# Performance work log

Measured on AMD Instinct MI355X. Metric: run time of the kernel, lower is better.

## Reference

```python
import jax, jax.numpy as jnp
import numpy as np


def _gcn_layer(h, src, dst, W, b, norm_src, norm_dst, n_nodes):
    # DGL GraphConv with norm='both': D_out^{-1/2} -> sum-aggregate -> D_in^{-1/2} -> XW + b
    m = (h * norm_src[:, None])[src]                       # [E, d] gather
    agg = jax.ops.segment_sum(m, dst, num_segments=n_nodes)  # [N, d] scatter-add
    return agg * norm_dst[:, None] @ W + b


def reference(features, src, dst, W1, b1, W2, b2):
    n_nodes = features.shape[0]
    ones = jnp.ones(src.shape[0], dtype=features.dtype)
    deg_out = jax.ops.segment_sum(ones, src, num_segments=n_nodes)
    deg_in = jax.ops.segment_sum(ones, dst, num_segments=n_nodes)
    # DGL clamps degrees to min 1 before the -1/2 power
    norm_src = jnp.clip(deg_out, 1.0, None) ** -0.5
    norm_dst = jnp.clip(deg_in, 1.0, None) ** -0.5

    h = jax.nn.relu(_gcn_layer(features, src, dst, W1, b1, norm_src, norm_dst, n_nodes))
    h = jax.nn.relu(_gcn_layer(h, src, dst, W2, b2, norm_src, norm_dst, n_nodes))
    return h


def setup_inputs() -> dict:
    key = jax.random.key(0)
    k1, k2, k3, k4, k5 = jax.random.split(key, 5)
    N, E, D = 50000, 600000, 128
    scale = 1.0 / np.sqrt(D)
    return {
        "features": jax.random.normal(k1, (N, D), dtype=jnp.float32),
        "src": jax.random.randint(k2, (E,), 0, N, dtype=jnp.int32),
        "dst": jax.random.randint(k3, (E,), 0, N, dtype=jnp.int32),
        "W1": jax.random.normal(k4, (D, D), dtype=jnp.float32) * scale,
        "b1": jnp.zeros((D,), dtype=jnp.float32),
        "W2": jax.random.normal(k5, (D, D), dtype=jnp.float32) * scale,
        "b2": jnp.zeros((D,), dtype=jnp.float32),
    }
```

## Files before the change

kernel.cpp:

```cpp
#include <hip/hip_runtime.h>

#define DIM 128
#define NCH 8
#define CH  22
#define HB  (NCH*CH)
#define HWORDS 25088
#define WSTR 136

typedef __attribute__((ext_vector_type(8))) short b8;
typedef __attribute__((ext_vector_type(4))) float f4;
typedef __attribute__((ext_vector_type(8))) unsigned short u16x8;

static __device__ __forceinline__ unsigned short f2bf(float f) {
    unsigned u = __float_as_uint(f);
    u += 0x7fffu + ((u >> 16) & 1u);
    return (unsigned short)(u >> 16);
}
static __device__ __forceinline__ float bf2f(unsigned short b) {
    return __uint_as_float((unsigned)b << 16);
}

__global__ __launch_bounds__(256) void k_hist(const int* __restrict__ src,
                                              const int* __restrict__ dst,
                                              unsigned short* __restrict__ local,
                                              unsigned* __restrict__ hist_in,
                                              unsigned* __restrict__ hist_out,
                                              int E, int W2p, int slice) {
    __shared__ unsigned h[HWORDS];
    const int t = threadIdx.x;
    const int b = blockIdx.x;
    const int e0 = b * slice;
    const int e1 = min(e0 + slice, E);
    const int W4 = W2p >> 2;
    uint4* h4 = (uint4*)h;

    for (int w = t; w < W4; w += 256) h4[w] = make_uint4(0u, 0u, 0u, 0u);
    __syncthreads();
    for (int e = e0 + t; e < e1; e += 256) {
        int d = dst[e];
        unsigned sh = (unsigned)(d & 1) * 16u;
        unsigned old = atomicAdd(&h[d >> 1], 1u << sh);
        local[e] = (unsigned short)((old >> sh) & 0xffffu);
    }
    __syncthreads();
    uint4* oin = (uint4*)(hist_in + (size_t)b * W2p);
    for (int w = t; w < W4; w += 256) { oin[w] = h4[w]; h4[w] = make_uint4(0u, 0u, 0u, 0u); }
    __syncthreads();
    for (int e = e0 + t; e < e1; e += 256) {
        int s = src[e];
        atomicAdd(&h[s >> 1], 1u << ((unsigned)(s & 1) * 16u));
    }
    __syncthreads();
    uint4* oout = (uint4*)(hist_out + (size_t)b * W2p);
    for (int w = t; w < W4; w += 256) oout[w] = h4[w];
}

__global__ __launch_bounds__(256) void k_colscan1(unsigned* __restrict__ hist_in,
                                                  const unsigned* __restrict__ hist_out,
                                                  unsigned* __restrict__ aux_in,
                                                  unsigned* __restrict__ aux_out,
                                                  int W2, int W2p) {
    int w = blockIdx.x * 256 + threadIdx.x;
    if (w >= W2) return;
    int ch = blockIdx.y;
    size_t base = (size_t)ch * CH * W2p + w;
    unsigned run = 0;
    #pragma unroll
    for (int b = 0; b < CH; ++b) {
        unsigned* p = hist_in + base + (size_t)b * W2p;
        unsigned x = *p;
        *p = run;
        run += x;
    }
    aux_in[(size_t)ch * W2p + w] = run;
    unsigned run2 = 0;
    #pragma unroll
    for (int b = 0; b < CH; ++b) run2 += hist_out[base + (size_t)b * W2p];
    aux_out[(size_t)ch * W2p + w] = run2;
}

__global__ __launch_bounds__(256) void k_colscan2(unsigned* __restrict__ aux_in,
                                                  const unsigned* __restrict__ aux_out,
                                                  int* __restrict__ cnt,
                                                  int* __restrict__ deg_out,
                                                  int* __restrict__ bsum,
                                                  int W2, int W2p, int N) {
    __shared__ int wsum[4];
    int w = blockIdx.x * 256 + threadIdx.x;
    unsigned run = 0, run2 = 0;
    if (w < W2) {
        #pragma unroll
        for (int ch = 0; ch < NCH; ++ch) {
            unsigned x = aux_in[(size_t)ch * W2p + w];
            aux_in[(size_t)ch * W2p + w] = run;
            run += x;
            run2 += aux_out[(size_t)ch * W2p + w];
        }
        int n0 = w * 2, n1 = n0 + 1;
        cnt[n0] = (int)(run & 0xffffu);
        deg_out[n0] = (int)(run2 & 0xffffu);
        if (n1 < N) {
            cnt[n1] = (int)(run >> 16);
            deg_out[n1] = (int)(run2 >> 16);
        } else {
            run &= 0xffffu;
        }
    }
    int tot = (int)(run & 0xffffu) + (int)(run >> 16);
    #pragma unroll
    for (int off = 32; off > 0; off >>= 1) tot += __shfl_down(tot, off, 64);
    int lane = threadIdx.x & 63, wave = threadIdx.x >> 6;
    if (lane == 0) wsum[wave] = tot;
    __syncthreads();
    if (threadIdx.x == 0)   bsum[2 * blockIdx.x]     = wsum[0] + wsum[1];
    if (threadIdx.x == 128) bsum[2 * blockIdx.x + 1] = wsum[2] + wsum[3];
}

__global__ __launch_bounds__(256) void k_edge_pass_fb(const int* __restrict__ src,
                                                      const int* __restrict__ dst,
                                                      int* __restrict__ deg_out,
                                                      int* __restrict__ cnt,
                                                      int* __restrict__ local_fb, int E) {
    int e = blockIdx.x * 256 + threadIdx.x;
    if (e < E) {
        atomicAdd(&deg_out[src[e]], 1);
        local_fb[e] = atomicAdd(&cnt[dst[e]], 1);
    }
}

__global__ __launch_bounds__(256) void k_block_reduce(const int* __restrict__ deg,
                                                      int* __restrict__ bsum, int N) {
    __shared__ int wsum[4];
    int i = blockIdx.x * 256 + threadIdx.x;
    int x = (i < N) ? deg[i] : 0;
    #pragma unroll
    for (int off = 32; off > 0; off >>= 1) x += __shfl_down(x, off, 64);
    int lane = threadIdx.x & 63, wave = threadIdx.x >> 6;
    if (lane == 0) wsum[wave] = x;
    __syncthreads();
    if (threadIdx.x == 0) bsum[blockIdx.x] = wsum[0] + wsum[1] + wsum[2] + wsum[3];
}

__global__ __launch_bounds__(256) void k_scan_final(const int* __restrict__ cnt,
                                                    const int* __restrict__ deg_out,
                                                    const int* __restrict__ bsum,
                                                    int* __restrict__ row_off,
                                                    float* __restrict__ norm_src,
                                                    float* __restrict__ norm_dst, int N) {
    __shared__ int wsum[4];
    __shared__ int base_s;
    const int t = threadIdx.x;
    const int lane = t & 63, wave = t >> 6;

    int pre = 0;
    for (int i = t; i < blockIdx.x; i += 256) pre += bsum[i];
    #pragma unroll
    for (int off = 32; off > 0; off >>= 1) pre += __shfl_down(pre, off, 64);
    if (lane == 0) wsum[wave] = pre;
    __syncthreads();
    if (t == 0) base_s = wsum[0] + wsum[1] + wsum[2] + wsum[3];
    __syncthreads();
    const int bpre_v = base_s;

    int i = blockIdx.x * 256 + t;
    int x = (i < N) ? cnt[i] : 0;
    int orig = x;
    #pragma unroll
    for (int off = 1; off < 64; off <<= 1) {
        int y = __shfl_up(x, off, 64);
        if (lane >= off) x += y;
    }
    if (lane == 63) wsum[wave] = x;
    __syncthreads();
    if (t == 0) {
        int s = 0;
        for (int w = 0; w < 4; ++w) { int tt = wsum[w]; wsum[w] = s; s += tt; }
    }
    __syncthreads();
    x += wsum[wave] + bpre_v;
    if (i < N) {
        row_off[i] = x - orig;
        int di = orig < 1 ? 1 : orig;
        norm_dst[i] = rsqrtf((float)di);
        int dov = deg_out[i]; if (dov < 1) dov = 1;
        norm_src[i] = rsqrtf((float)dov);
    }
    if (i == N - 1) row_off[N] = x;
}

__global__ __launch_bounds__(256) void k_fill_cast_prep(
        const int* __restrict__ src, const int* __restrict__ dst,
        const int* __restrict__ row_off,
        const unsigned short* __restrict__ local,
        const int* __restrict__ local_fb,
        const unsigned* __restrict__ hist_in,
        const unsigned* __restrict__ aux_in,
        int* __restrict__ csr_src,
        const float* __restrict__ feat, const float* __restrict__ norm_src,
        unsigned short* __restrict__ fbf,
        const float* __restrict__ W1, const float* __restrict__ W2,
        unsigned short* __restrict__ w1hi, unsigned short* __restrict__ w1lo,
        unsigned short* __restrict__ w2hi, unsigned short* __restrict__ w2lo,
        int E, int W2p, int slice, int eb, int cb, int pb, int n4) {
    int bx = blockIdx.x;
    if (bx < eb) {
        int e = bx * 256 + threadIdx.x;
        if (e < E) {
            int d = dst[e];
            int pos = row_off[d];
            if (hist_in) {
                int b = e / slice;
                int ch = b / CH;
                unsigned sh = (unsigned)(d & 1) * 16u;
                unsigned bo = (hist_in[(size_t)b * W2p + (d >> 1)] >> sh) & 0xffffu;
                unsigned cbs = (aux_in[(size_t)ch * W2p + (d >> 1)] >> sh) & 0xffffu;
                pos += (int)bo + (int)cbs + (int)local[e];
            } else {
                pos += local_fb[e];
            }
            csr_src[pos] = src[e];
        }
    } else if (bx < eb + cb) {
        int i = (bx - eb) * 256 + threadIdx.x;
        if (i < n4) {
            float4 v = ((const float4*)feat)[i];
            float ns = norm_src[i >> 5];
            ushort4 o;
            o.x = f2bf(v.x * ns); o.y = f2bf(v.y * ns);
            o.z = f2bf(v.z * ns); o.w = f2bf(v.w * ns);
            ((ushort4*)fbf)[i] = o;
        }
    } else {
        int b = bx - eb - cb;
        const float* W; unsigned short *Hi, *Lo;
        if (b < pb) { W = W1; Hi = w1hi; Lo = w1lo; } else { W = W2; Hi = w2hi; Lo = w2lo; b -= pb; }
        int e = b * 256 + threadIdx.x;
        if (e < DIM * DIM) {
            int k = e >> 7, c = e & 127;
            float w = W[e];
            unsigned short hi = f2bf(w);
            unsigned short lo = f2bf(w - bf2f(hi));
            Hi[c * DIM + k] = hi;
            Lo[c * DIM + k] = lo;
        }
    }
}

__global__ __launch_bounds__(256) void k_spmm(const unsigned short* __restrict__ hb,
                                              const int* __restrict__ csr_src,
                                              const int* __restrict__ row_off,
                                              const float* __restrict__ norm_dst,
                                              unsigned short* __restrict__ aggbf, int N) {
    int t = blockIdx.x * 256 + threadIdx.x;
    int node = t >> 4;
    int lane = t & 15;
    if (node >= N) return;
    int beg = row_off[node], end = row_off[node + 1];
    float a0[8] = {0.f, 0.f, 0.f, 0.f, 0.f, 0.f, 0.f, 0.f};
    float a1[8] = {0.f, 0.f, 0.f, 0.f, 0.f, 0.f, 0.f, 0.f};
    int i = beg;
    for (; i + 4 <= end; i += 4) {
        int s0 = csr_src[i], s1 = csr_src[i + 1], s2 = csr_src[i + 2], s3 = csr_src[i + 3];
        u16x8 u0 = *((const u16x8*)(hb + (size_t)s0 * DIM) + lane);
        u16x8 u1 = *((const u16x8*)(hb + (size_t)s1 * DIM) + lane);
        u16x8 u2 = *((const u16x8*)(hb + (size_t)s2 * DIM) + lane);
        u16x8 u3 = *((const u16x8*)(hb + (size_t)s3 * DIM) + lane);
        #pragma unroll
        for (int j = 0; j < 8; ++j) {
            a0[j] += bf2f(u0[j]);
            a1[j] += bf2f(u1[j]);
            a0[j] += bf2f(u2[j]);
            a1[j] += bf2f(u3[j]);
        }
    }
    for (; i < end; ++i) {
        int s0 = csr_src[i];
        u16x8 u0 = *((const u16x8*)(hb + (size_t)s0 * DIM) + lane);
        #pragma unroll
        for (int j = 0; j < 8; ++j) a0[j] += bf2f(u0[j]);
    }
    float nd = norm_dst[node];
    u16x8 o;
    #pragma unroll
    for (int j = 0; j < 8; ++j) o[j] = f2bf((a0[j] + a1[j]) * nd);
    *((u16x8*)(aggbf + (size_t)node * DIM) + lane) = o;
}

__global__ __launch_bounds__(256, 2) void k_gemm_mfma(
        const unsigned short* __restrict__ A,
        const unsigned short* __restrict__ Wt_hi,
        const unsigned short* __restrict__ Wt_lo,
        const float* __restrict__ bias,
        const float* __restrict__ postscale,
        float* __restrict__ outf, unsigned short* __restrict__ outbf, int N) {
    __shared__ unsigned short WH[DIM * WSTR];
    __shared__ unsigned short WL[DIM * WSTR];

    const int t = threadIdx.x;
    #pragma unroll
    for (int i = 0; i < 8; ++i) {
        int e = (t + i * 256) * 8;
        int c = e >> 7, k = e & 127;
        *(float4*)(WH + c * WSTR + k) = *(const float4*)(Wt_hi + e);
        *(float4*)(WL + c * WSTR + k) = *(const float4*)(Wt_lo + e);
    }
    __syncthreads();

    const int wv = t >> 6;
    const int l = t & 63;
    const int m = l & 15;
    const int quad = l >> 4;
    const int row_t0 = blockIdx.x * 128 + wv * 32;

    f4 acc[2][8];
    #pragma unroll
    for (int rt = 0; rt < 2; ++rt)
        #pragma unroll
        for (int ct = 0; ct < 8; ++ct)
            acc[rt][ct] = (f4){0.f, 0.f, 0.f, 0.f};

    int r0 = row_t0 + m;      if (r0 >= N) r0 = N - 1;
    int r1 = row_t0 + 16 + m; if (r1 >= N) r1 = N - 1;

    #pragma unroll
    for (int ks = 0; ks < 4; ++ks) {
        int koff = ks * 32 + quad * 8;
        b8 a0 = *(const b8*)(A + (size_t)r0 * DIM + koff);
        b8 a1 = *(const b8*)(A + (size_t)r1 * DIM + koff);
        #pragma unroll
        for (int ct = 0; ct < 8; ++ct) {
            int c = ct * 16 + m;
            b8 bh = *(const b8*)(WH + c * WSTR + koff);
            b8 bl = *(const b8*)(WL + c * WSTR + koff);
            acc[0][ct] = __builtin_amdgcn_mfma_f32_16x16x32_bf16(a0, bh, acc[0][ct], 0, 0, 0);
            acc[0][ct] = __builtin_amdgcn_mfma_f32_16x16x32_bf16(a0, bl, acc[0][ct], 0, 0, 0);
            acc[1][ct] = __builtin_amdgcn_mfma_f32_16x16x32_bf16(a1, bh, acc[1][ct], 0, 0, 0);
            acc[1][ct] = __builtin_amdgcn_mfma_f32_16x16x32_bf16(a1, bl, acc[1][ct], 0, 0, 0);
        }
    }

    #pragma unroll
    for (int rt = 0; rt < 2; ++rt) {
        int rowb = row_t0 + rt * 16 + quad * 4;
        #pragma unroll
        for (int r = 0; r < 4; ++r) {
            int gr = rowb + r;
            if (gr < N) {
                float s = postscale ? postscale[gr] : 1.f;
                #pragma unroll
                for (int ct = 0; ct < 8; ++ct) {
                    int col = ct * 16 + m;
                    float v = fmaxf(acc[rt][ct][r] + bias[col], 0.f) * s;
                    if (outbf) outbf[(size_t)gr * DIM + col] = f2bf(v);
                    else       outf[(size_t)gr * DIM + col] = v;
                }
            }
        }
    }
}

static inline size_t align_up(size_t x, size_t a) { return (x + a - 1) & ~(a - 1); }

extern "C" void kernel_launch(void* const* d_in, const int* in_sizes, int n_in,
                              void* d_out, int out_size, void* d_ws, size_t ws_size,
                              hipStream_t stream) {
    const float* features = (const float*)d_in[0];
    const int*   src      = (const int*)d_in[1];
    const int*   dst      = (const int*)d_in[2];
    const float* W1       = (const float*)d_in[3];
    const float* b1       = (const float*)d_in[4];
    const float* W2       = (const float*)d_in[5];
    const float* b2       = (const float*)d_in[6];
    float* out = (float*)d_out;

    const int N = in_sizes[0] / DIM;
    const int E = in_sizes[1];
    const int B = (N + 255) / 256;
    const int W2w = (N + 1) >> 1;
    const int W2p = (W2w + 3) & ~3;
    const int slice = (E + HB - 1) / HB;
    const int cs_blocks = (W2w + 255) / 256;

    size_t nodeb = align_up((size_t)N * 4, 256);
    char* p = (char*)d_ws;
    int*   deg_out  = (int*)p;                      p += nodeb;
    int*   cnt      = (int*)p;                      p += nodeb;
    float* norm_src = (float*)p;                    p += nodeb;
    float* norm_dst = (float*)p;                    p += nodeb;
    int*   row_off  = (int*)p;                      p += align_up((size_t)(N + 1) * 4, 256);
    int*   bsum     = (int*)p;                      p += align_up((size_t)(2 * cs_blocks) * 4, 256);
    int*   csr_src  = (int*)p;                      p += align_up((size_t)E * 4, 256);
    char*  big      = p;                            p += 2 * (size_t)N * DIM * 4;
    unsigned short* w1hi = (unsigned short*)p;      p += (size_t)DIM * DIM * 2;
    unsigned short* w1lo = (unsigned short*)p;      p += (size_t)DIM * DIM * 2;
    unsigned short* w2hi = (unsigned short*)p;      p += (size_t)DIM * DIM * 2;
    unsigned short* w2lo = (unsigned short*)p;      p += (size_t)DIM * DIM * 2;
    unsigned short* aggbf = (unsigned short*)big;
    unsigned short* h1bf  = (unsigned short*)(big + (size_t)N * DIM * 2);
    unsigned short* fbf   = (unsigned short*)(big + 3 * (size_t)N * DIM * 2);
    char* ap = big;
    unsigned short* local = (unsigned short*)ap;    ap += align_up((size_t)E * 2, 256);
    unsigned* hist_in  = (unsigned*)ap;             ap += (size_t)HB * W2p * 4;
    unsigned* hist_out = (unsigned*)ap;             ap += (size_t)HB * W2p * 4;
    unsigned* aux_in   = (unsigned*)ap;             ap += (size_t)NCH * W2p * 4;
    unsigned* aux_out  = (unsigned*)ap;             ap += (size_t)NCH * W2p * 4;
    int* local_fb = (int*)big;

    const int edge_blocks = (E + 255) / 256;
    const int spmm_blocks = (int)(((size_t)N * 16 + 255) / 256);
    const int gemm_blocks = (N + 127) / 128;
    const int n4 = N * (DIM / 4);
    const int cast_blocks = (n4 + 255) / 256;
    const int prep_blocks = (DIM * DIM + 255) / 256;
    const int fcp_blocks  = edge_blocks + cast_blocks + 2 * prep_blocks;

    const bool fast = (W2p <= HWORDS) &&
        (align_up((size_t)E * 2, 256) + (2 * (size_t)HB + 2 * NCH) * W2p * 4
            <= 3 * (size_t)N * DIM * 2);

    if (fast) {
        k_hist<<<HB, 256, 0, stream>>>(src, dst, local, hist_in, hist_out, E, W2p, slice);
        k_colscan1<<<dim3(cs_blocks, NCH), 256, 0, stream>>>(hist_in, hist_out, aux_in, aux_out, W2w, W2p);
        k_colscan2<<<cs_blocks, 256, 0, stream>>>(aux_in, aux_out, cnt, deg_out, bsum, W2w, W2p, N);
        k_scan_final<<<B, 256, 0, stream>>>(cnt, deg_out, bsum, row_off, norm_src, norm_dst, N);
        k_fill_cast_prep<<<fcp_blocks, 256, 0, stream>>>(
            src, dst, row_off, local, (const int*)nullptr, hist_in, aux_in, csr_src,
            features, norm_src, fbf, W1, W2, w1hi, w1lo, w2hi, w2lo,
            E, W2p, slice, edge_blocks, cast_blocks, prep_blocks, n4);
    } else {
        hipMemsetAsync(deg_out, 0, nodeb * 2, stream);
        k_edge_pass_fb<<<edge_blocks, 256, 0, stream>>>(src, dst, deg_out, cnt, local_fb, E);
        k_block_reduce<<<B, 256, 0, stream>>>(cnt, bsum, N);
        k_scan_final<<<B, 256, 0, stream>>>(cnt, deg_out, bsum, row_off, norm_src, norm_dst, N);
        k_fill_cast_prep<<<fcp_blocks, 256, 0, stream>>>(
            src, dst, row_off, (const unsigned short*)nullptr, local_fb,
            (const unsigned*)nullptr, (const unsigned*)nullptr, csr_src,
            features, norm_src, fbf, W1, W2, w1hi, w1lo, w2hi, w2lo,
            E, W2p, slice, edge_blocks, cast_blocks, prep_blocks, n4);
    }

    k_spmm<<<spmm_blocks, 256, 0, stream>>>(fbf, csr_src, row_off, norm_dst, aggbf, N);
    k_gemm_mfma<<<gemm_blocks, 256, 0, stream>>>(aggbf, w1hi, w1lo, b1, norm_src,
                                                 (float*)nullptr, h1bf, N);

    k_spmm<<<spmm_blocks, 256, 0, stream>>>(h1bf, csr_src, row_off, norm_dst, aggbf, N);
    k_gemm_mfma<<<gemm_blocks, 256, 0, stream>>>(aggbf, w2hi, w2lo, b2, (const float*)nullptr,
                                                 out, (unsigned short*)nullptr, N);
}
```

Measured before the change: 218.3 us.

## Simplify CSR build: fewer histogram blocks, global packed out-degree atomics, single column scan

Measured after the change: 238.8 us. 1.09x slower.

```diff
diff --git a/kernel.cpp b/kernel.cpp
--- a/kernel.cpp
+++ b/kernel.cpp
@@ -1,9 +1,7 @@
 #include <hip/hip_runtime.h>
 
 #define DIM 128
-#define NCH 8
-#define CH  22
-#define HB  (NCH*CH)
+#define HB  96
 #define HWORDS 25088
 #define WSTR 136
 
@@ -24,7 +22,7 @@
                                               const int* __restrict__ dst,
                                               unsigned short* __restrict__ local,
                                               unsigned* __restrict__ hist_in,
-                                              unsigned* __restrict__ hist_out,
+                                              unsigned* __restrict__ degp,
                                               int E, int W2p, int slice) {
     __shared__ unsigned h[HWORDS];
     const int t = threadIdx.x;
@@ -38,71 +36,38 @@
     __syncthreads();
     for (int e = e0 + t; e < e1; e += 256) {
         int d = dst[e];
+        int s = src[e];
         unsigned sh = (unsigned)(d & 1) * 16u;
         unsigned old = atomicAdd(&h[d >> 1], 1u << sh);
         local[e] = (unsigned short)((old >> sh) & 0xffffu);
+        atomicAdd(&degp[s >> 1], 1u << ((unsigned)(s & 1) * 16u));
     }
     __syncthreads();
     uint4* oin = (uint4*)(hist_in + (size_t)b * W2p);
-    for (int w = t; w < W4; w += 256) { oin[w] = h4[w]; h4[w] = make_uint4(0u, 0u, 0u, 0u); }
-    __syncthreads();
-    for (int e = e0 + t; e < e1; e += 256) {
-        int s = src[e];
-        atomicAdd(&h[s >> 1], 1u << ((unsigned)(s & 1) * 16u));
-    }
-    __syncthreads();
-    uint4* oout = (uint4*)(hist_out + (size_t)b * W2p);
-    for (int w = t; w < W4; w += 256) oout[w] = h4[w];
-}
-
-__global__ __launch_bounds__(256) void k_colscan1(unsigned* __restrict__ hist_in,
-                                                  const unsigned* __restrict__ hist_out,
-                                                  unsigned* __restrict__ aux_in,
-                                                  unsigned* __restrict__ aux_out,
-                                                  int W2, int W2p) {
-    int w = blockIdx.x * 256 + threadIdx.x;
-    if (w >= W2) return;
-    int ch = blockIdx.y;
-    size_t base = (size_t)ch * CH * W2p + w;
-    unsigned run = 0;
-    #pragma unroll
-    for (int b = 0; b < CH; ++b) {
-        unsigned* p = hist_in + base + (size_t)b * W2p;
-        unsigned x = *p;
-        *p = run;
-        run += x;
-    }
-    aux_in[(size_t)ch * W2p + w] = run;
-    unsigned run2 = 0;
-    #pragma unroll
-    for (int b = 0; b < CH; ++b) run2 += hist_out[base + (size_t)b * W2p];
-    aux_out[(size_t)ch * W2p + w] = run2;
-}
-
-__global__ __launch_bounds__(256) void k_colscan2(unsigned* __restrict__ aux_in,
-                                                  const unsigned* __restrict__ aux_out,
-                                                  int* __restrict__ cnt,
-                                                  int* __restrict__ deg_out,
-                                                  int* __restrict__ bsum,
-                                                  int W2, int W2p, int N) {
+    for (int w = t; w < W4; w += 256) oin[w] = h4[w];
+}
+
+__global__ __launch_bounds__(256) void k_colscan(unsigned* __restrict__ hist_in,
+                                                 int* __restrict__ cnt,
+                                                 int* __restrict__ bsum,
+                                                 int W2, int W2p, int N) {
     __shared__ int wsum[4];
     int w = blockIdx.x * 256 + threadIdx.x;
-    unsigned run = 0, run2 = 0;
+    unsigned run = 0;
     if (w < W2) {
-        #pragma unroll
-        for (int ch = 0; ch < NCH; ++ch) {
-            unsigned x = aux_in[(size_t)ch * W2p + w];
-            aux_in[(size_t)ch * W2p + w] = run;
+        unsigned* p = hist_in + w;
+        #pragma unroll 8
+        for (int b = 0; b < HB; ++b) {
+            unsigned x = *p;
+            *p = run;
             run += x;
-            run2 += aux_out[(size_t)ch * W2p + w];
-        }
-        int n0 = w * 2, n1 = n0 + 1;
-        cnt[n0] = (int)(run & 0xffffu);
-        deg_out[n0] = (int)(run2 & 0xffffu);
-        if (n1 < N) {
-            cnt[n1] = (int)(run >> 16);
-            deg_out[n1] = (int)(run2 >> 16);
+            p += W2p;
+        }
+        int n0 = w * 2;
+        if (n0 + 1 < N) {
+            *(int2*)(cnt + n0) = make_int2((int)(run & 0xffffu), (int)(run >> 16));
         } else {
+            cnt[n0] = (int)(run & 0xffffu);
             run &= 0xffffu;
         }
     }
@@ -142,7 +107,8 @@
 }
 
 __global__ __launch_bounds__(256) void k_scan_final(const int* __restrict__ cnt,
-                                                    const int* __restrict__ deg_out,
+                                                    const unsigned* __restrict__ degp,
+                                                    const int* __restrict__ deg_fb,
                                                     const int* __restrict__ bsum,
                                                     int* __restrict__ row_off,
                                                     float* __restrict__ norm_src,
@@ -182,7 +148,14 @@
         row_off[i] = x - orig;
         int di = orig < 1 ? 1 : orig;
         norm_dst[i] = rsqrtf((float)di);
-        int dov = deg_out[i]; if (dov < 1) dov = 1;
+        int dov;
+        if (degp) {
+            unsigned dw = degp[(unsigned)i >> 1];
+            dov = (int)((dw >> ((unsigned)(i & 1) * 16u)) & 0xffffu);
+        } else {
+            dov = deg_fb[i];
+        }
+        if (dov < 1) dov = 1;
         norm_src[i] = rsqrtf((float)dov);
     }
     if (i == N - 1) row_off[N] = x;
@@ -194,7 +167,6 @@
         const unsigned short* __restrict__ local,
         const int* __restrict__ local_fb,
         const unsigned* __restrict__ hist_in,
-        const unsigned* __restrict__ aux_in,
         int* __restrict__ csr_src,
         const float* __restrict__ feat, const float* __restrict__ norm_src,
         unsigned short* __restrict__ fbf,
@@ -210,11 +182,9 @@
             int pos = row_off[d];
             if (hist_in) {
                 int b = e / slice;
-                int ch = b / CH;
                 unsigned sh = (unsigned)(d & 1) * 16u;
                 unsigned bo = (hist_in[(size_t)b * W2p + (d >> 1)] >> sh) & 0xffffu;
-                unsigned cbs = (aux_in[(size_t)ch * W2p + (d >> 1)] >> sh) & 0xffffu;
-                pos += (int)bo + (int)cbs + (int)local[e];
+                pos += (int)bo + (int)local[e];
             } else {
                 pos += local_fb[e];
             }
@@ -401,9 +371,6 @@
     char* ap = big;
     unsigned short* local = (unsigned short*)ap;    ap += align_up((size_t)E * 2, 256);
     unsigned* hist_in  = (unsigned*)ap;             ap += (size_t)HB * W2p * 4;
-    unsigned* hist_out = (unsigned*)ap;             ap += (size_t)HB * W2p * 4;
-    unsigned* aux_in   = (unsigned*)ap;             ap += (size_t)NCH * W2p * 4;
-    unsigned* aux_out  = (unsigned*)ap;             ap += (size_t)NCH * W2p * 4;
     int* local_fb = (int*)big;
 
     const int edge_blocks = (E + 255) / 256;
@@ -415,26 +382,28 @@
     const int fcp_blocks  = edge_blocks + cast_blocks + 2 * prep_blocks;
 
     const bool fast = (W2p <= HWORDS) &&
-        (align_up((size_t)E * 2, 256) + (2 * (size_t)HB + 2 * NCH) * W2p * 4
+        (align_up((size_t)E * 2, 256) + (size_t)HB * W2p * 4
             <= 3 * (size_t)N * DIM * 2);
 
     if (fast) {
-        k_hist<<<HB, 256, 0, stream>>>(src, dst, local, hist_in, hist_out, E, W2p, slice);
-        k_colscan1<<<dim3(cs_blocks, NCH), 256, 0, stream>>>(hist_in, hist_out, aux_in, aux_out, W2w, W2p);
-        k_colscan2<<<cs_blocks, 256, 0, stream>>>(aux_in, aux_out, cnt, deg_out, bsum, W2w, W2p, N);
-        k_scan_final<<<B, 256, 0, stream>>>(cnt, deg_out, bsum, row_off, norm_src, norm_dst, N);
+        hipMemsetAsync(deg_out, 0, (size_t)W2p * 4, stream);
+        k_hist<<<HB, 256, 0, stream>>>(src, dst, local, hist_in, (unsigned*)deg_out, E, W2p, slice);
+        k_colscan<<<cs_blocks, 256, 0, stream>>>(hist_in, cnt, bsum, W2w, W2p, N);
+        k_scan_final<<<B, 256, 0, stream>>>(cnt, (const unsigned*)deg_out, (const int*)nullptr,
+                                            bsum, row_off, norm_src, norm_dst, N);
         k_fill_cast_prep<<<fcp_blocks, 256, 0, stream>>>(
-            src, dst, row_off, local, (const int*)nullptr, hist_in, aux_in, csr_src,
+            src, dst, row_off, local, (const int*)nullptr, hist_in, csr_src,
             features, norm_src, fbf, W1, W2, w1hi, w1lo, w2hi, w2lo,
             E, W2p, slice, edge_blocks, cast_blocks, prep_blocks, n4);
     } else {
         hipMemsetAsync(deg_out, 0, nodeb * 2, stream);
         k_edge_pass_fb<<<edge_blocks, 256, 0, stream>>>(src, dst, deg_out, cnt, local_fb, E);
         k_block_reduce<<<B, 256, 0, stream>>>(cnt, bsum, N);
-        k_scan_final<<<B, 256, 0, stream>>>(cnt, deg_out, bsum, row_off, norm_src, norm_dst, N);
+        k_scan_final<<<B, 256, 0, stream>>>(cnt, (const unsigned*)nullptr, deg_out,
+                                            bsum, row_off, norm_src, norm_dst, N);
         k_fill_cast_prep<<<fcp_blocks, 256, 0, stream>>>(
             src, dst, row_off, (const unsigned short*)nullptr, local_fb,
-            (const unsigned*)nullptr, (const unsigned*)nullptr, csr_src,
+            (const unsigned*)nullptr, csr_src,
             features, norm_src, fbf, W1, W2, w1hi, w1lo, w2hi, w2lo,
             E, W2p, slice, edge_blocks, cast_blocks, prep_blocks, n4);
     }
```
